# Performance work log

Measured on AMD Instinct MI355X. Metric: run time of the kernel, lower is better.

Reference implementation:

```python
import jax, jax.numpy as jnp
import numpy as np

B, C, H, W = 16, 512, 32, 32
HW = H * W  # == input_features == output_features for shapes to be consistent


def setup_inputs() -> dict:
    key = jax.random.key(0)
    k1, k2, k3 = jax.random.split(key, 3)
    node1 = jax.random.normal(k1, (B, C, H, W), dtype=jnp.float32)
    node2 = jax.random.normal(k2, (B, C, H, W), dtype=jnp.float32)
    # nn.Linear(input_features, output_features, bias=False).weight: [out, in]
    W_c = jax.random.normal(k3, (HW, HW), dtype=jnp.float32) * (1.0 / np.sqrt(HW))
    return {"node1": node1, "node2": node2, "W_c": W_c}


def reference(node1, node2, W_c):
    b, c, h, w = node1.shape
    hw = h * w
    n1 = node1.reshape(b, c, hw)  # [B, C, HW]
    n2 = node2.reshape(b, c, hw)  # [B, C, HW]
    # x = W_c(n1): Linear applies y = x @ W^T  -> [B, C, HW_out]
    x = jnp.einsum('bch,oh->bco', n1, W_c)
    # e = bmm(x.permute(0,2,1), n2): [B, HW_out, C] @ [B, C, HW] -> [B, HW_out, HW]
    e = jnp.einsum('bco,bch->boh', x, n2)
    a = jax.nn.softmax(e, axis=-1)  # softmax over last dim (HW of node2)
    # m = bmm(n2, a): [B, C, HW] @ [B, HW, HW] -> [B, C, HW]
    m = jnp.einsum('bck,bkj->bcj', n2, a)
    return m
```

## Files before the change

kernel.cpp:

```cpp
#include <hip/hip_runtime.h>
#include <math.h>


typedef _Float16 f16;
typedef _Float16 f16x8 __attribute__((ext_vector_type(8)));
typedef _Float16 f16x4 __attribute__((ext_vector_type(4)));
typedef float f32x4 __attribute__((ext_vector_type(4)));

#define L2E 1.442695040888963f

#define WG_BARRIER() asm volatile("s_waitcnt lgkmcnt(0)\ns_barrier" ::: "memory")

__global__ __launch_bounds__(256) void prep(const float* __restrict__ n1,
                                            const float* __restrict__ Wc,
                                            const float* __restrict__ n2,
                                            f16* __restrict__ n1f, f16* __restrict__ Wf,
                                            f16* __restrict__ n2f, f16* __restrict__ n2t) {
    const int bid = blockIdx.x, tid = threadIdx.x;
    if (bid < 4608) {
        const float* s = (bid < 4096) ? n1 : Wc;
        f16* d = (bid < 4096) ? n1f : Wf;
        const size_t i = ((size_t)(bid < 4096 ? bid : bid - 4096) * 256 + tid) * 8;
        f32x4 a = *(const f32x4*)(s + i);
        f32x4 b = *(const f32x4*)(s + i + 4);
        f16x8 o;
        o[0] = (f16)a[0]; o[1] = (f16)a[1]; o[2] = (f16)a[2]; o[3] = (f16)a[3];
        o[4] = (f16)b[0]; o[5] = (f16)b[1]; o[6] = (f16)b[2]; o[7] = (f16)b[3];
        *(f16x8*)(d + i) = o;
        return;
    }
    const int id = bid - 4608;
    const int b = id >> 7;
    const int ry = (id & 127) >> 4;
    const int cx = id & 15;
    const float* S = n2 + (size_t)b * 512 * 1024;
    f16* Dn = n2f + (size_t)b * 512 * 1024;
    f16* Dt = n2t + (size_t)b * 1024 * 512;
    __shared__ f16 Ts[64 * 72];
    const int r0 = ry * 64, c0 = cx * 64;
    const int rr = tid >> 3, cc8 = (tid & 7) * 8;
#pragma unroll
    for (int h = 0; h < 2; ++h) {
        const int row = r0 + rr + 32 * h;
        const float* s = S + (size_t)row * 1024 + c0 + cc8;
        f32x4 a = *(const f32x4*)s, bq = *(const f32x4*)(s + 4);
        f16x8 o;
        o[0] = (f16)a[0]; o[1] = (f16)a[1]; o[2] = (f16)a[2]; o[3] = (f16)a[3];
        o[4] = (f16)bq[0]; o[5] = (f16)bq[1]; o[6] = (f16)bq[2]; o[7] = (f16)bq[3];
        *(f16x8*)&Ts[(rr + 32 * h) * 72 + cc8] = o;
        *(f16x8*)(Dn + (size_t)row * 1024 + c0 + cc8) = o;
    }
    __syncthreads();
    const int j = tid >> 2, k16 = (tid & 3) * 16;
    f16* d = Dt + (size_t)(c0 + j) * 512 + r0 + k16;
    f16x8 o0, o1;
#pragma unroll
    for (int i = 0; i < 8; ++i) {
        o0[i] = Ts[(k16 + i) * 72 + j];
        o1[i] = Ts[(k16 + 8 + i) * 72 + j];
    }
    *(f16x8*)d = o0;
    *(f16x8*)(d + 8) = o1;
}

__global__ __launch_bounds__(256) void stats_partial(const f16* __restrict__ Et,
                                                     float* __restrict__ Pm,
                                                     float* __restrict__ Ps) {
    const int b = blockIdx.x & 15, chunk = blockIdx.x >> 4;
    const int half = threadIdx.x >> 7;
    const int t = threadIdx.x & 127;
    const f16* p = Et + (size_t)b * 1024 * 1024 +
                   ((size_t)chunk * 64 + half * 32) * 1024 + t * 8;
    float m[8], s[8];
#pragma unroll
    for (int c = 0; c < 8; ++c) { m[c] = -3.0e38f; s[c] = 0.f; }
#pragma unroll 4
    for (int j = 0; j < 32; ++j) {
        f16x8 v8 = *(const f16x8*)(p + (size_t)j * 1024);
#pragma unroll
        for (int c = 0; c < 8; ++c) {
            float v = (float)v8[c];
            float nm = fmaxf(m[c], v);
            s[c] = s[c] * __expf(m[c] - nm) + __expf(v - nm);
            m[c] = nm;
        }
    }
    const int idx32 = b * 32 + chunk * 2 + half;
    f32x4 mo0, mo1, so0, so1;
#pragma unroll
    for (int c = 0; c < 4; ++c) { mo0[c] = m[c]; mo1[c] = m[c + 4];
                                  so0[c] = s[c]; so1[c] = s[c + 4]; }
    float* pmo = Pm + (size_t)idx32 * 1024 + t * 8;
    float* pso = Ps + (size_t)idx32 * 1024 + t * 8;
    *(f32x4*)pmo = mo0; *(f32x4*)(pmo + 4) = mo1;
    *(f32x4*)pso = so0; *(f32x4*)(pso + 4) = so1;
}

__global__ __launch_bounds__(256) void stats_combine(const float* __restrict__ Pm,
                                                     const float* __restrict__ Ps,
                                                     float* __restrict__ Sc) {
    const int g = blockIdx.x * 256 + threadIdx.x;
    const int b = g >> 10, o = g & 1023;
    const float* pm = Pm + (size_t)b * 32 * 1024 + o;
    const float* ps = Ps + (size_t)b * 32 * 1024 + o;
    float M = -3.0e38f;
#pragma unroll
    for (int c = 0; c < 32; ++c) M = fmaxf(M, pm[c * 1024]);
    float S = 0.f;
#pragma unroll
    for (int c = 0; c < 32; ++c) S += ps[c * 1024] * __expf(pm[c * 1024] - M);
    Sc[g] = (M + __logf(S)) * L2E;
}

#define GEMM_CORE_D2(NS)                                                                \
    f16x8 pa0 = *(const f16x8*)gAp, pb0 = *(const f16x8*)gBp;                           \
    *(f16x8*)wA0 = pa0; *(f16x8*)wB0 = pb0;                                             \
    f16x8 pa1 = *(const f16x8*)(gAp + 64), pb1 = *(const f16x8*)(gBp + 64);             \
    pa0 = *(const f16x8*)(gAp + 128); pb0 = *(const f16x8*)(gBp + 128);                 \
    WG_BARRIER();                                                                       \
    f32x4 acc[4][2] = {};                                                               \
_Pragma("unroll")                                                                       \
    for (int kb = 0; kb < (NS); ++kb) {                                                 \
        const char* Ac = SM + (kb & 1) * 10240;                                         \
        const char* Bc = SM + 20480 + (kb & 1) * 10240;                                 \
        f16x8 fa[4], fb[2];                                                             \
_Pragma("unroll")                                                                       \
        for (int u = 0; u < 4; ++u)                                                     \
            fa[u] = *(const f16x8*)(Ac + (wm + u * 16 + col) * 80 + quad * 16);         \
_Pragma("unroll")                                                                       \
        for (int v = 0; v < 2; ++v)                                                     \
            fb[v] = *(const f16x8*)(Bc + (wn + v * 16 + col) * 80 + quad * 16);         \
_Pragma("unroll")                                                                       \
        for (int u = 0; u < 4; ++u)                                                     \
_Pragma("unroll")                                                                       \
            for (int v = 0; v < 2; ++v)                                                 \
                acc[u][v] = __builtin_amdgcn_mfma_f32_16x16x32_f16(fa[u], fb[v],        \
                                                                   acc[u][v], 0, 0, 0);\
        if (kb + 1 < (NS)) {                                                            \
            char* dA = SM + ((kb + 1) & 1) * 10240 + sOff;                              \
            char* dB = SM + 20480 + ((kb + 1) & 1) * 10240 + sOff;                      \
            if ((kb & 1) == 0) {                                                        \
                *(f16x8*)dA = pa1; *(f16x8*)dB = pb1;                                   \
                if (kb + 3 < (NS)) {                                                    \
                    pa1 = *(const f16x8*)(gAp + (size_t)(kb + 3) * 64);                 \
                    pb1 = *(const f16x8*)(gBp + (size_t)(kb + 3) * 64);                 \
                }                                                                       \
            } else {                                                                    \
                *(f16x8*)dA = pa0; *(f16x8*)dB = pb0;                                   \
                if (kb + 3 < (NS)) {                                                    \
                    pa0 = *(const f16x8*)(gAp + (size_t)(kb + 3) * 64);                 \
                    pb0 = *(const f16x8*)(gBp + (size_t)(kb + 3) * 64);                 \
                }                                                                       \
            }                                                                           \
            WG_BARRIER();                                                               \
        }                                                                               \
    }

__global__ __launch_bounds__(512) void gemm1_nt_xt(const f16* __restrict__ A,
                                                   const f16* __restrict__ Bw,
                                                   f16* __restrict__ Xt) {
    const int M = 512, K = 1024;
    const int id = blockIdx.x;
    const int xcd = id & 7, loc = id >> 3;
    const int b = xcd * 2 + (loc >> 5);
    const int m0 = ((loc >> 3) & 3) * 128;
    const int n0 = (loc & 7) * 128;
    A += (size_t)b * M * K;
    Xt += (size_t)b * 1024 * M;
    __shared__ __attribute__((aligned(16))) char SM[40960];
    const int tid = threadIdx.x, lane = tid & 63, wave = tid >> 6;
    const int col = lane & 15, quad = lane >> 4;
    const int wm = (wave & 1) * 64, wn = (wave >> 1) * 32;
    const int srow = wave * 16 + (lane >> 2), scolb = (lane & 3) * 16;
    const int sOff = srow * 80 + scolb;
    const char* gAp = (const char*)A + (size_t)(m0 + srow) * K * 2 + scolb;
    const char* gBp = (const char*)Bw + (size_t)(n0 + srow) * K * 2 + scolb;
    char* wA0 = SM + sOff;
    char* wB0 = SM + 20480 + sOff;

    GEMM_CORE_D2(32)

    WG_BARRIER();
    f16* Tt = (f16*)SM;
#pragma unroll
    for (int u = 0; u < 4; ++u)
#pragma unroll
        for (int v = 0; v < 2; ++v) {
            f16x4 p;
#pragma unroll
            for (int r = 0; r < 4; ++r) p[r] = (f16)acc[u][v][r];
            *(f16x4*)&Tt[(wn + v * 16 + col) * 136 + wm + u * 16 + quad * 4] = p;
        }
    WG_BARRIER();
    const int j = tid >> 2, seg = (tid & 3) * 32;
    f16* dst = Xt + (size_t)(n0 + j) * M + m0 + seg;
#pragma unroll
    for (int c8 = 0; c8 < 32; c8 += 8)
        *(f16x8*)(dst + c8) = *(const f16x8*)&Tt[j * 136 + seg + c8];
}

__global__ __launch_bounds__(512) void gemm2_nt_et(const f16* __restrict__ A,
                                                   const f16* __restrict__ B,
                                                   f16* __restrict__ Et) {
    const int K = 512;
    const int id = blockIdx.x;
    const int xcd = id & 7, loc = id >> 3;
    const int b = xcd * 2 + (loc >> 6);
    const int m0 = ((loc >> 3) & 7) * 128;
    const int n0 = (loc & 7) * 128;
    A += (size_t)b * 1024 * K;
    B += (size_t)b * 1024 * K;
    Et += (size_t)b * 1024 * 1024;
    __shared__ __attribute__((aligned(16))) char SM[40960];
    const int tid = threadIdx.x, lane = tid & 63, wave = tid >> 6;
    const int col = lane & 15, quad = lane >> 4;
    const int wm = (wave & 1) * 64, wn = (wave >> 1) * 32;
    const int srow = wave * 16 + (lane >> 2), scolb = (lane & 3) * 16;
    const int sOff = srow * 80 + scolb;
    const char* gAp = (const char*)A + (size_t)(m0 + srow) * K * 2 + scolb;
    const char* gBp = (const char*)B + (size_t)(n0 + srow) * K * 2 + scolb;
    char* wA0 = SM + sOff;
    char* wB0 = SM + 20480 + sOff;

    GEMM_CORE_D2(16)

    WG_BARRIER();
    f16* Tt = (f16*)SM;
#pragma unroll
    for (int u = 0; u < 4; ++u)
#pragma unroll
        for (int v = 0; v < 2; ++v) {
            f16x4 p;
#pragma unroll
            for (int r = 0; r < 4; ++r) p[r] = (f16)acc[u][v][r];
            *(f16x4*)&Tt[(wn + v * 16 + col) * 136 + wm + u * 16 + quad * 4] = p;
        }
    WG_BARRIER();
    const int j = tid >> 2, seg = (tid & 3) * 32;
    f16* dst = Et + (size_t)(n0 + j) * 1024 + m0 + seg;
#pragma unroll
    for (int c8 = 0; c8 < 32; c8 += 8)
        *(f16x8*)(dst + c8) = *(const f16x8*)&Tt[j * 136 + seg + c8];
}

__global__ __launch_bounds__(512) void gemm3_nt_out(const f16* __restrict__ A,
                                                    const f16* __restrict__ Et,
                                                    const float* __restrict__ Sc,
                                                    float* __restrict__ C) {
    const int K = 1024, NS = 32;
    const int id = blockIdx.x;
    const int xcd = id & 7, loc = id >> 3;
    const int b = xcd * 2 + (loc >> 5);
    const int m0 = ((loc >> 3) & 3) * 128;
    const int n0 = (loc & 7) * 128;
    A += (size_t)b * 512 * K;
    Et += (size_t)b * 1024 * K;
    Sc += (size_t)b * 1024;
    C += (size_t)b * 512 * 1024;
    __shared__ __attribute__((aligned(16))) char SM[40960];
    const int tid = threadIdx.x, lane = tid & 63, wave = tid >> 6;
    const int col = lane & 15, quad = lane >> 4;
    const int wm = (wave & 1) * 64, wn = (wave >> 1) * 32;
    const int srow = wave * 16 + (lane >> 2), scolb = (lane & 3) * 16;
    const int sOff = srow * 80 + scolb;
    const char* gAp = (const char*)A + (size_t)(m0 + srow) * K * 2 + scolb;
    const char* gBp = (const char*)Et + (size_t)(n0 + srow) * K * 2 + scolb;
    const float* gSp = Sc + (scolb >> 1);
    char* wA0 = SM + sOff;
    char* wB0 = SM + 20480 + sOff;

    f16x8 pa0 = *(const f16x8*)gAp, pb0 = *(const f16x8*)gBp;
    f32x4 c00 = *(const f32x4*)gSp, c01 = *(const f32x4*)(gSp + 4);
    {
        f16x8 rbs;
#pragma unroll
        for (int i = 0; i < 4; ++i)
            rbs[i] = (f16)exp2f(fmaf((float)pb0[i], L2E, -c00[i]));
#pragma unroll
        for (int i = 0; i < 4; ++i)
            rbs[4 + i] = (f16)exp2f(fmaf((float)pb0[4 + i], L2E, -c01[i]));
        *(f16x8*)wA0 = pa0;
        *(f16x8*)wB0 = rbs;
    }
    f16x8 pa1 = *(const f16x8*)(gAp + 64), pb1 = *(const f16x8*)(gBp + 64);
    f32x4 c10 = *(const f32x4*)(gSp + 32), c11 = *(const f32x4*)(gSp + 36);
    pa0 = *(const f16x8*)(gAp + 128); pb0 = *(const f16x8*)(gBp + 128);
    c00 = *(const f32x4*)(gSp + 64); c01 = *(const f32x4*)(gSp + 68);
    WG_BARRIER();
    f32x4 acc[4][2] = {};
#pragma unroll
    for (int kb = 0; kb < NS; ++kb) {
        const char* Ac = SM + (kb & 1) * 10240;
        const char* Bc = SM + 20480 + (kb & 1) * 10240;
        f16x8 fa[4], fb[2];
#pragma unroll
        for (int u = 0; u < 4; ++u)
            fa[u] = *(const f16x8*)(Ac + (wm + u * 16 + col) * 80 + quad * 16);
#pragma unroll
        for (int v = 0; v < 2; ++v)
            fb[v] = *(const f16x8*)(Bc + (wn + v * 16 + col) * 80 + quad * 16);
#pragma unroll
        for (int u = 0; u < 4; ++u)
#pragma unroll
            for (int v = 0; v < 2; ++v)
                acc[u][v] = __builtin_amdgcn_mfma_f32_16x16x32_f16(fa[u], fb[v],
                                                                   acc[u][v], 0, 0, 0);
        if (kb + 1 < NS) {
            char* dA = SM + ((kb + 1) & 1) * 10240 + sOff;
            char* dB = SM + 20480 + ((kb + 1) & 1) * 10240 + sOff;
            f16x8 rbs;
            if ((kb & 1) == 0) {
#pragma unroll
                for (int i = 0; i < 4; ++i)
                    rbs[i] = (f16)exp2f(fmaf((float)pb1[i], L2E, -c10[i]));
#pragma unroll
                for (int i = 0; i < 4; ++i)
                    rbs[4 + i] = (f16)exp2f(fmaf((float)pb1[4 + i], L2E, -c11[i]));
                *(f16x8*)dA = pa1;
                *(f16x8*)dB = rbs;
                if (kb + 3 < NS) {
                    pa1 = *(const f16x8*)(gAp + (size_t)(kb + 3) * 64);
                    pb1 = *(const f16x8*)(gBp + (size_t)(kb + 3) * 64);
                    c10 = *(const f32x4*)(gSp + (size_t)(kb + 3) * 32);
                    c11 = *(const f32x4*)(gSp + (size_t)(kb + 3) * 32 + 4);
                }
            } else {
#pragma unroll
                for (int i = 0; i < 4; ++i)
                    rbs[i] = (f16)exp2f(fmaf((float)pb0[i], L2E, -c00[i]));
#pragma unroll
                for (int i = 0; i < 4; ++i)
                    rbs[4 + i] = (f16)exp2f(fmaf((float)pb0[4 + i], L2E, -c01[i]));
                *(f16x8*)dA = pa0;
                *(f16x8*)dB = rbs;
                if (kb + 3 < NS) {
                    pa0 = *(const f16x8*)(gAp + (size_t)(kb + 3) * 64);
                    pb0 = *(const f16x8*)(gBp + (size_t)(kb + 3) * 64);
                    c00 = *(const f32x4*)(gSp + (size_t)(kb + 3) * 32);
                    c01 = *(const f32x4*)(gSp + (size_t)(kb + 3) * 32 + 4);
                }
            }
            WG_BARRIER();
        }
    }

#pragma unroll
    for (int u = 0; u < 4; ++u)
#pragma unroll
        for (int v = 0; v < 2; ++v)
#pragma unroll
            for (int r = 0; r < 4; ++r)
                C[(size_t)(m0 + wm + u * 16 + quad * 4 + r) * 1024 + n0 + wn + v * 16 + col] =
                    acc[u][v][r];
}

extern "C" void kernel_launch(void* const* d_in, const int* in_sizes, int n_in,
                              void* d_out, int out_size, void* d_ws, size_t ws_size,
                              hipStream_t stream) {
    const float* n1 = (const float*)d_in[0];
    const float* n2 = (const float*)d_in[1];
    const float* Wc = (const float*)d_in[2];
    float* out = (float*)d_out;
    char* ws = (char*)d_ws;

    f16* n2t = (f16*)(ws);
    f16* Xt  = (f16*)(ws + (16u << 20));
    f16* Wf  = (f16*)(ws + (32u << 20));
    f16* Et  = (f16*)(ws + (32u << 20));
    f16* n1f = (f16*)(ws + (64u << 20));
    f16* n2f = (f16*)(ws + (80u << 20));
    float* Pm = (float*)(ws + (64u << 20));
    float* Ps = (float*)(ws + (66u << 20));
    float* Sc = (float*)(ws + (68u << 20));

    prep<<<6656, dim3(256), 0, stream>>>(n1, Wc, n2, n1f, Wf, n2f, n2t);
    gemm1_nt_xt<<<512, dim3(512), 0, stream>>>(n1f, Wf, Xt);
    gemm2_nt_et<<<1024, dim3(512), 0, stream>>>(Xt, n2t, Et);
    stats_partial<<<256, dim3(256), 0, stream>>>(Et, Pm, Ps);
    stats_combine<<<64, dim3(256), 0, stream>>>(Pm, Ps, Sc);
    gemm3_nt_out<<<512, dim3(512), 0, stream>>>(n2f, Et, Sc, out);
}
```

Before: 218.0 us.

## Enlarge GEMM tiles to 256x128 with swizzled LDS layout in shared core

The three GEMM kernels now use 256x128 output tiles per workgroup (each wave computes 64x64) instead of 128x128, halving the grid sizes. The padded 80-byte LDS rows are replaced by 64-byte rows with an XOR swizzle to avoid bank conflicts, and the GEMM main loop becomes a shared template with an optional exp-on-load path for the softmax GEMM. The aim is more data reuse per LDS load and fewer global reads per FLOP. The cost is fewer workgroups (256 for gemm1/gemm3, which may underfill the GPU), more accumulator registers per thread, and a two-pass transposed epilogue.

```diff
diff --git a/kernel.cpp b/kernel.cpp
--- a/kernel.cpp
+++ b/kernel.cpp
@@ -112,91 +112,146 @@
     Sc[g] = (M + __logf(S)) * L2E;
 }
 
-#define GEMM_CORE_D2(NS)                                                                \
-    f16x8 pa0 = *(const f16x8*)gAp, pb0 = *(const f16x8*)gBp;                           \
-    *(f16x8*)wA0 = pa0; *(f16x8*)wB0 = pb0;                                             \
-    f16x8 pa1 = *(const f16x8*)(gAp + 64), pb1 = *(const f16x8*)(gBp + 64);             \
-    pa0 = *(const f16x8*)(gAp + 128); pb0 = *(const f16x8*)(gBp + 128);                 \
-    WG_BARRIER();                                                                       \
-    f32x4 acc[4][2] = {};                                                               \
-_Pragma("unroll")                                                                       \
-    for (int kb = 0; kb < (NS); ++kb) {                                                 \
-        const char* Ac = SM + (kb & 1) * 10240;                                         \
-        const char* Bc = SM + 20480 + (kb & 1) * 10240;                                 \
-        f16x8 fa[4], fb[2];                                                             \
-_Pragma("unroll")                                                                       \
-        for (int u = 0; u < 4; ++u)                                                     \
-            fa[u] = *(const f16x8*)(Ac + (wm + u * 16 + col) * 80 + quad * 16);         \
-_Pragma("unroll")                                                                       \
-        for (int v = 0; v < 2; ++v)                                                     \
-            fb[v] = *(const f16x8*)(Bc + (wn + v * 16 + col) * 80 + quad * 16);         \
-_Pragma("unroll")                                                                       \
-        for (int u = 0; u < 4; ++u)                                                     \
-_Pragma("unroll")                                                                       \
-            for (int v = 0; v < 2; ++v)                                                 \
-                acc[u][v] = __builtin_amdgcn_mfma_f32_16x16x32_f16(fa[u], fb[v],        \
-                                                                   acc[u][v], 0, 0, 0);\
-        if (kb + 1 < (NS)) {                                                            \
-            char* dA = SM + ((kb + 1) & 1) * 10240 + sOff;                              \
-            char* dB = SM + 20480 + ((kb + 1) & 1) * 10240 + sOff;                      \
-            if ((kb & 1) == 0) {                                                        \
-                *(f16x8*)dA = pa1; *(f16x8*)dB = pb1;                                   \
-                if (kb + 3 < (NS)) {                                                    \
-                    pa1 = *(const f16x8*)(gAp + (size_t)(kb + 3) * 64);                 \
-                    pb1 = *(const f16x8*)(gBp + (size_t)(kb + 3) * 64);                 \
-                }                                                                       \
-            } else {                                                                    \
-                *(f16x8*)dA = pa0; *(f16x8*)dB = pb0;                                   \
-                if (kb + 3 < (NS)) {                                                    \
-                    pa0 = *(const f16x8*)(gAp + (size_t)(kb + 3) * 64);                 \
-                    pb0 = *(const f16x8*)(gBp + (size_t)(kb + 3) * 64);                 \
-                }                                                                       \
-            }                                                                           \
-            WG_BARRIER();                                                               \
-        }                                                                               \
-    }
+__device__ __forceinline__ f16x8 expb(f16x8 b, f32x4 cl, f32x4 ch) {
+    f16x8 t;
+#pragma unroll
+    for (int i = 0; i < 4; ++i) t[i] = (f16)exp2f(fmaf((float)b[i], L2E, -cl[i]));
+#pragma unroll
+    for (int i = 0; i < 4; ++i) t[4 + i] = (f16)exp2f(fmaf((float)b[4 + i], L2E, -ch[i]));
+    return t;
+}
+
+template <int NS, bool EXPB>
+__device__ __forceinline__ void gemm_core(const char* gA0, const char* gA1,
+                                          const char* gB, const float* gSp,
+                                          char* SM, int sOff, int wm, int wn,
+                                          int col, int swz16, f32x4 (&acc)[4][4]) {
+    f16x8 a00 = *(const f16x8*)gA0, a01 = *(const f16x8*)gA1;
+    f16x8 b0 = *(const f16x8*)gB;
+    f32x4 c00, c01, c10, c11;
+    if (EXPB) { c00 = *(const f32x4*)gSp; c01 = *(const f32x4*)(gSp + 4); }
+    {
+        char* dA = SM + sOff;
+        *(f16x8*)dA = a00;
+        *(f16x8*)(dA + 8192) = a01;
+        char* dB = SM + 32768 + sOff;
+        *(f16x8*)dB = EXPB ? expb(b0, c00, c01) : b0;
+    }
+    f16x8 a10 = *(const f16x8*)(gA0 + 64), a11 = *(const f16x8*)(gA1 + 64);
+    f16x8 b1 = *(const f16x8*)(gB + 64);
+    if (EXPB) { c10 = *(const f32x4*)(gSp + 32); c11 = *(const f32x4*)(gSp + 36); }
+    a00 = *(const f16x8*)(gA0 + 128); a01 = *(const f16x8*)(gA1 + 128);
+    b0 = *(const f16x8*)(gB + 128);
+    if (EXPB) { c00 = *(const f32x4*)(gSp + 64); c01 = *(const f32x4*)(gSp + 68); }
+    WG_BARRIER();
+#pragma unroll
+    for (int kb = 0; kb < NS; ++kb) {
+        const char* Ac = SM + (kb & 1) * 16384;
+        const char* Bc = SM + 32768 + (kb & 1) * 8192;
+        f16x8 fa[4], fb[4];
+#pragma unroll
+        for (int u = 0; u < 4; ++u)
+            fa[u] = *(const f16x8*)(Ac + (wm + u * 16 + col) * 64 + swz16);
+#pragma unroll
+        for (int v = 0; v < 4; ++v)
+            fb[v] = *(const f16x8*)(Bc + (wn + v * 16 + col) * 64 + swz16);
+#pragma unroll
+        for (int u = 0; u < 4; ++u)
+#pragma unroll
+            for (int v = 0; v < 4; ++v)
+                acc[u][v] = __builtin_amdgcn_mfma_f32_16x16x32_f16(fa[u], fb[v],
+                                                                   acc[u][v], 0, 0, 0);
+        if (kb + 1 < NS) {
+            char* dA = SM + ((kb + 1) & 1) * 16384 + sOff;
+            char* dB = SM + 32768 + ((kb + 1) & 1) * 8192 + sOff;
+            if ((kb & 1) == 0) {
+                *(f16x8*)dA = a10;
+                *(f16x8*)(dA + 8192) = a11;
+                *(f16x8*)dB = EXPB ? expb(b1, c10, c11) : b1;
+                if (kb + 3 < NS) {
+                    a10 = *(const f16x8*)(gA0 + (size_t)(kb + 3) * 64);
+                    a11 = *(const f16x8*)(gA1 + (size_t)(kb + 3) * 64);
+                    b1 = *(const f16x8*)(gB + (size_t)(kb + 3) * 64);
+                    if (EXPB) {
+                        c10 = *(const f32x4*)(gSp + (size_t)(kb + 3) * 32);
+                        c11 = *(const f32x4*)(gSp + (size_t)(kb + 3) * 32 + 4);
+                    }
+                }
+            } else {
+                *(f16x8*)dA = a00;
+                *(f16x8*)(dA + 8192) = a01;
+                *(f16x8*)dB = EXPB ? expb(b0, c00, c01) : b0;
+                if (kb + 3 < NS) {
+                    a00 = *(const f16x8*)(gA0 + (size_t)(kb + 3) * 64);
+                    a01 = *(const f16x8*)(gA1 + (size_t)(kb + 3) * 64);
+                    b0 = *(const f16x8*)(gB + (size_t)(kb + 3) * 64);
+                    if (EXPB) {
+                        c00 = *(const f32x4*)(gSp + (size_t)(kb + 3) * 32);
+                        c01 = *(const f32x4*)(gSp + (size_t)(kb + 3) * 32 + 4);
+                    }
+                }
+            }
+            WG_BARRIER();
+        }
+    }
+}
+
+__device__ __forceinline__ void epilogue_tr(f32x4 (&acc)[4][4], char* SM, f16* dst0,
+                                            int dstRow, int m0, int n0, int tid) {
+    const int lane = tid & 63, wave = tid >> 6;
+    const int col = lane & 15, quad = lane >> 4;
+    const int wn = (wave >> 2) * 64;
+    const int mh_w = (wave >> 1) & 1;
+    const int wm_loc = (wave & 1) * 64;
+    const int j = tid >> 2, seg = (tid & 3) * 32;
+    WG_BARRIER();
+    f16* Tt = (f16*)SM;
+#pragma unroll
+    for (int mh = 0; mh < 2; ++mh) {
+        if (mh_w == mh) {
+#pragma unroll
+            for (int u = 0; u < 4; ++u)
+#pragma unroll
+                for (int v = 0; v < 4; ++v) {
+                    f16x4 p;
+#pragma unroll
+                    for (int r = 0; r < 4; ++r) p[r] = (f16)acc[u][v][r];
+                    *(f16x4*)&Tt[(wn + v * 16 + col) * 136 + wm_loc + u * 16 + quad * 4] = p;
+                }
+        }
+        WG_BARRIER();
+        f16* dst = dst0 + (size_t)(n0 + j) * dstRow + m0 + mh * 128 + seg;
+#pragma unroll
+        for (int c8 = 0; c8 < 32; c8 += 8)
+            *(f16x8*)(dst + c8) = *(const f16x8*)&Tt[j * 136 + seg + c8];
+        if (mh == 0) WG_BARRIER();
+    }
+}
 
 __global__ __launch_bounds__(512) void gemm1_nt_xt(const f16* __restrict__ A,
                                                    const f16* __restrict__ Bw,
                                                    f16* __restrict__ Xt) {
-    const int M = 512, K = 1024;
+    const int K = 1024;
     const int id = blockIdx.x;
     const int xcd = id & 7, loc = id >> 3;
-    const int b = xcd * 2 + (loc >> 5);
-    const int m0 = ((loc >> 3) & 3) * 128;
+    const int b = xcd * 2 + (loc >> 4);
+    const int m0 = ((loc >> 3) & 1) * 256;
     const int n0 = (loc & 7) * 128;
-    A += (size_t)b * M * K;
-    Xt += (size_t)b * 1024 * M;
-    __shared__ __attribute__((aligned(16))) char SM[40960];
+    A += (size_t)b * 512 * K;
+    Xt += (size_t)b * 1024 * 512;
+    __shared__ __attribute__((aligned(16))) char SM[49152];
     const int tid = threadIdx.x, lane = tid & 63, wave = tid >> 6;
     const int col = lane & 15, quad = lane >> 4;
-    const int wm = (wave & 1) * 64, wn = (wave >> 1) * 32;
-    const int srow = wave * 16 + (lane >> 2), scolb = (lane & 3) * 16;
-    const int sOff = srow * 80 + scolb;
-    const char* gAp = (const char*)A + (size_t)(m0 + srow) * K * 2 + scolb;
-    const char* gBp = (const char*)Bw + (size_t)(n0 + srow) * K * 2 + scolb;
-    char* wA0 = SM + sOff;
-    char* wB0 = SM + 20480 + sOff;
-
-    GEMM_CORE_D2(32)
-
-    WG_BARRIER();
-    f16* Tt = (f16*)SM;
-#pragma unroll
-    for (int u = 0; u < 4; ++u)
-#pragma unroll
-        for (int v = 0; v < 2; ++v) {
-            f16x4 p;
-#pragma unroll
-            for (int r = 0; r < 4; ++r) p[r] = (f16)acc[u][v][r];
-            *(f16x4*)&Tt[(wn + v * 16 + col) * 136 + wm + u * 16 + quad * 4] = p;
-        }
-    WG_BARRIER();
-    const int j = tid >> 2, seg = (tid & 3) * 32;
-    f16* dst = Xt + (size_t)(n0 + j) * M + m0 + seg;
-#pragma unroll
-    for (int c8 = 0; c8 < 32; c8 += 8)
-        *(f16x8*)(dst + c8) = *(const f16x8*)&Tt[j * 136 + seg + c8];
+    const int wm = (wave & 3) * 64, wn = (wave >> 2) * 64;
+    const int srow = tid >> 2, sslot = tid & 3;
+    const int sOff = srow * 64 + ((sslot ^ ((srow >> 1) & 3)) * 16);
+    const int swz16 = (quad ^ ((col >> 1) & 3)) * 16;
+    const char* gA0 = (const char*)A + (size_t)(m0 + srow) * K * 2 + sslot * 16;
+    const char* gA1 = gA0 + (size_t)128 * K * 2;
+    const char* gB = (const char*)Bw + (size_t)(n0 + srow) * K * 2 + sslot * 16;
+    f32x4 acc[4][4] = {};
+    gemm_core<32, false>(gA0, gA1, gB, nullptr, SM, sOff, wm, wn, col, swz16, acc);
+    epilogue_tr(acc, SM, Xt, 512, m0, n0, tid);
 }
 
 __global__ __launch_bounds__(512) void gemm2_nt_et(const f16* __restrict__ A,
@@ -205,149 +260,59 @@
     const int K = 512;
     const int id = blockIdx.x;
     const int xcd = id & 7, loc = id >> 3;
-    const int b = xcd * 2 + (loc >> 6);
-    const int m0 = ((loc >> 3) & 7) * 128;
+    const int b = xcd * 2 + (loc >> 5);
+    const int m0 = ((loc >> 3) & 3) * 256;
     const int n0 = (loc & 7) * 128;
     A += (size_t)b * 1024 * K;
     B += (size_t)b * 1024 * K;
     Et += (size_t)b * 1024 * 1024;
-    __shared__ __attribute__((aligned(16))) char SM[40960];
+    __shared__ __attribute__((aligned(16))) char SM[49152];
     const int tid = threadIdx.x, lane = tid & 63, wave = tid >> 6;
     const int col = lane & 15, quad = lane >> 4;
-    const int wm = (wave & 1) * 64, wn = (wave >> 1) * 32;
-    const int srow = wave * 16 + (lane >> 2), scolb = (lane & 3) * 16;
-    const int sOff = srow * 80 + scolb;
-    const char* gAp = (const char*)A + (size_t)(m0 + srow) * K * 2 + scolb;
-    const char* gBp = (const char*)B + (size_t)(n0 + srow) * K * 2 + scolb;
-    char* wA0 = SM + sOff;
-    char* wB0 = SM + 20480 + sOff;
-
-    GEMM_CORE_D2(16)
-
-    WG_BARRIER();
-    f16* Tt = (f16*)SM;
-#pragma unroll
-    for (int u = 0; u < 4; ++u)
-#pragma unroll
-        for (int v = 0; v < 2; ++v) {
-            f16x4 p;
-#pragma unroll
-            for (int r = 0; r < 4; ++r) p[r] = (f16)acc[u][v][r];
-            *(f16x4*)&Tt[(wn + v * 16 + col) * 136 + wm + u * 16 + quad * 4] = p;
-        }
-    WG_BARRIER();
-    const int j = tid >> 2, seg = (tid & 3) * 32;
-    f16* dst = Et + (size_t)(n0 + j) * 1024 + m0 + seg;
-#pragma unroll
-    for (int c8 = 0; c8 < 32; c8 += 8)
-        *(f16x8*)(dst + c8) = *(const f16x8*)&Tt[j * 136 + seg + c8];
+    const int wm = (wave & 3) * 64, wn = (wave >> 2) * 64;
+    const int srow = tid >> 2, sslot = tid & 3;
+    const int sOff = srow * 64 + ((sslot ^ ((srow >> 1) & 3)) * 16);
+    const int swz16 = (quad ^ ((col >> 1) & 3)) * 16;
+    const char* gA0 = (const char*)A + (size_t)(m0 + srow) * K * 2 + sslot * 16;
+    const char* gA1 = gA0 + (size_t)128 * K * 2;
+    const char* gB = (const char*)B + (size_t)(n0 + srow) * K * 2 + sslot * 16;
+    f32x4 acc[4][4] = {};
+    gemm_core<16, false>(gA0, gA1, gB, nullptr, SM, sOff, wm, wn, col, swz16, acc);
+    epilogue_tr(acc, SM, Et, 1024, m0, n0, tid);
 }
 
 __global__ __launch_bounds__(512) void gemm3_nt_out(const f16* __restrict__ A,
                                                     const f16* __restrict__ Et,
                                                     const float* __restrict__ Sc,
                                                     float* __restrict__ C) {
-    const int K = 1024, NS = 32;
+    const int K = 1024;
     const int id = blockIdx.x;
     const int xcd = id & 7, loc = id >> 3;
-    const int b = xcd * 2 + (loc >> 5);
-    const int m0 = ((loc >> 3) & 3) * 128;
+    const int b = xcd * 2 + (loc >> 4);
+    const int m0 = ((loc >> 3) & 1) * 256;
     const int n0 = (loc & 7) * 128;
     A += (size_t)b * 512 * K;
     Et += (size_t)b * 1024 * K;
     Sc += (size_t)b * 1024;
     C += (size_t)b * 512 * 1024;
-    __shared__ __attribute__((aligned(16))) char SM[40960];
+    __shared__ __attribute__((aligned(16))) char SM[49152];
     const int tid = threadIdx.x, lane = tid & 63, wave = tid >> 6;
     const int col = lane & 15, quad = lane >> 4;
-    const int wm = (wave & 1) * 64, wn = (wave >> 1) * 32;
-    const int srow = wave * 16 + (lane >> 2), scolb = (lane & 3) * 16;
-    const int sOff = srow * 80 + scolb;
-    const char* gAp = (const char*)A + (size_t)(m0 + srow) * K * 2 + scolb;
-    const char* gBp = (const char*)Et + (size_t)(n0 + srow) * K * 2 + scolb;
-    const float* gSp = Sc + (scolb >> 1);
-    char* wA0 = SM + sOff;
-    char* wB0 = SM + 20480 + sOff;
-
-    f16x8 pa0 = *(const f16x8*)gAp, pb0 = *(const f16x8*)gBp;
-    f32x4 c00 = *(const f32x4*)gSp, c01 = *(const f32x4*)(gSp + 4);
-    {
-        f16x8 rbs;
-#pragma unroll
-        for (int i = 0; i < 4; ++i)
-            rbs[i] = (f16)exp2f(fmaf((float)pb0[i], L2E, -c00[i]));
-#pragma unroll
-        for (int i = 0; i < 4; ++i)
-            rbs[4 + i] = (f16)exp2f(fmaf((float)pb0[4 + i], L2E, -c01[i]));
-        *(f16x8*)wA0 = pa0;
-        *(f16x8*)wB0 = rbs;
-    }
-    f16x8 pa1 = *(const f16x8*)(gAp + 64), pb1 = *(const f16x8*)(gBp + 64);
-    f32x4 c10 = *(const f32x4*)(gSp + 32), c11 = *(const f32x4*)(gSp + 36);
-    pa0 = *(const f16x8*)(gAp + 128); pb0 = *(const f16x8*)(gBp + 128);
-    c00 = *(const f32x4*)(gSp + 64); c01 = *(const f32x4*)(gSp + 68);
-    WG_BARRIER();
-    f32x4 acc[4][2] = {};
-#pragma unroll
-    for (int kb = 0; kb < NS; ++kb) {
-        const char* Ac = SM + (kb & 1) * 10240;
-        const char* Bc = SM + 20480 + (kb & 1) * 10240;
-        f16x8 fa[4], fb[2];
-#pragma unroll
-        for (int u = 0; u < 4; ++u)
-            fa[u] = *(const f16x8*)(Ac + (wm + u * 16 + col) * 80 + quad * 16);
-#pragma unroll
-        for (int v = 0; v < 2; ++v)
-            fb[v] = *(const f16x8*)(Bc + (wn + v * 16 + col) * 80 + quad * 16);
-#pragma unroll
-        for (int u = 0; u < 4; ++u)
-#pragma unroll
-            for (int v = 0; v < 2; ++v)
-                acc[u][v] = __builtin_amdgcn_mfma_f32_16x16x32_f16(fa[u], fb[v],
-                                                                   acc[u][v], 0, 0, 0);
-        if (kb + 1 < NS) {
-            char* dA = SM + ((kb + 1) & 1) * 10240 + sOff;
-            char* dB = SM + 20480 + ((kb + 1) & 1) * 10240 + sOff;
-            f16x8 rbs;
-            if ((kb & 1) == 0) {
-#pragma unroll
-                for (int i = 0; i < 4; ++i)
-                    rbs[i] = (f16)exp2f(fmaf((float)pb1[i], L2E, -c10[i]));
-#pragma unroll
-                for (int i = 0; i < 4; ++i)
-                    rbs[4 + i] = (f16)exp2f(fmaf((float)pb1[4 + i], L2E, -c11[i]));
-                *(f16x8*)dA = pa1;
-                *(f16x8*)dB = rbs;
-                if (kb + 3 < NS) {
-                    pa1 = *(const f16x8*)(gAp + (size_t)(kb + 3) * 64);
-                    pb1 = *(const f16x8*)(gBp + (size_t)(kb + 3) * 64);
-                    c10 = *(const f32x4*)(gSp + (size_t)(kb + 3) * 32);
-                    c11 = *(const f32x4*)(gSp + (size_t)(kb + 3) * 32 + 4);
-                }
-            } else {
-#pragma unroll
-                for (int i = 0; i < 4; ++i)
-                    rbs[i] = (f16)exp2f(fmaf((float)pb0[i], L2E, -c00[i]));
-#pragma unroll
-                for (int i = 0; i < 4; ++i)
-                    rbs[4 + i] = (f16)exp2f(fmaf((float)pb0[4 + i], L2E, -c01[i]));
-                *(f16x8*)dA = pa0;
-                *(f16x8*)dB = rbs;
-                if (kb + 3 < NS) {
-                    pa0 = *(const f16x8*)(gAp + (size_t)(kb + 3) * 64);
-                    pb0 = *(const f16x8*)(gBp + (size_t)(kb + 3) * 64);
-                    c00 = *(const f32x4*)(gSp + (size_t)(kb + 3) * 32);
-                    c01 = *(const f32x4*)(gSp + (size_t)(kb + 3) * 32 + 4);
-                }
-            }
-            WG_BARRIER();
-        }
-    }
+    const int wm = (wave & 3) * 64, wn = (wave >> 2) * 64;
+    const int srow = tid >> 2, sslot = tid & 3;
+    const int sOff = srow * 64 + ((sslot ^ ((srow >> 1) & 3)) * 16);
+    const int swz16 = (quad ^ ((col >> 1) & 3)) * 16;
+    const char* gA0 = (const char*)A + (size_t)(m0 + srow) * K * 2 + sslot * 16;
+    const char* gA1 = gA0 + (size_t)128 * K * 2;
+    const char* gB = (const char*)Et + (size_t)(n0 + srow) * K * 2 + sslot * 16;
+    const float* gSp = Sc + sslot * 8;
+    f32x4 acc[4][4] = {};
+    gemm_core<32, true>(gA0, gA1, gB, gSp, SM, sOff, wm, wn, col, swz16, acc);
 
 #pragma unroll
     for (int u = 0; u < 4; ++u)
 #pragma unroll
-        for (int v = 0; v < 2; ++v)
+        for (int v = 0; v < 4; ++v)
 #pragma unroll
             for (int r = 0; r < 4; ++r)
                 C[(size_t)(m0 + wm + u * 16 + quad * 4 + r) * 1024 + n0 + wn + v * 16 + col] =
@@ -374,9 +339,9 @@
     float* Sc = (float*)(ws + (68u << 20));
 
     prep<<<6656, dim3(256), 0, stream>>>(n1, Wc, n2, n1f, Wf, n2f, n2t);
-    gemm1_nt_xt<<<512, dim3(512), 0, stream>>>(n1f, Wf, Xt);
-    gemm2_nt_et<<<1024, dim3(512), 0, stream>>>(Xt, n2t, Et);
+    gemm1_nt_xt<<<256, dim3(512), 0, stream>>>(n1f, Wf, Xt);
+    gemm2_nt_et<<<512, dim3(512), 0, stream>>>(Xt, n2t, Et);
     stats_partial<<<256, dim3(256), 0, stream>>>(Et, Pm, Ps);
     stats_combine<<<64, dim3(256), 0, stream>>>(Pm, Ps, Sc);
-    gemm3_nt_out<<<512, dim3(512), 0, stream>>>(n2f, Et, Sc, out);
-}
+    gemm3_nt_out<<<256, dim3(512), 0, stream>>>(n2f, Et, Sc, out);
+}
```

Result: faster. 205.1 us (-5.9%).
